# Optimization experiments

Measured on AMD Instinct MI355X. Metric: run time of the kernel, lower is better.

Reference implementation:

```python
import jax, jax.numpy as jnp
import numpy as np

B, S, D = 4, 2048, 1024
N_HEAD = 16
HEAD_DIM = D // N_HEAD


def setup_inputs() -> dict:
    key = jax.random.key(0)
    k1, k2, k3 = jax.random.split(key, 3)
    std = 0.02
    return {
        "x": jax.random.normal(k1, (B, S, D), dtype=jnp.float32),
        "c_attn_w": jax.random.normal(k2, (D, 3 * D), dtype=jnp.float32) * std,
        "c_attn_b": jnp.zeros((3 * D,), dtype=jnp.float32),
        "c_proj_w": jax.random.normal(k3, (D, D), dtype=jnp.float32) * std,
        "c_proj_b": jnp.zeros((D,), dtype=jnp.float32),
    }


def _split_heads(t):
    # [B, S, D] -> [B, H, S, hd]
    b, s, d = t.shape
    return t.reshape(b, s, N_HEAD, d // N_HEAD).transpose(0, 2, 1, 3)


def reference(x, c_attn_w, c_attn_b, c_proj_w, c_proj_b):
    # fused QKV projection (TFConv1D = x @ w + b)
    qkv = x @ c_attn_w + c_attn_b                      # [B, S, 3D]
    q, k, v = jnp.split(qkv, 3, axis=2)
    q, k, v = _split_heads(q), _split_heads(k), _split_heads(v)  # [B, H, S, hd]

    # scaled scores
    w = jnp.einsum('bhqd,bhkd->bhqk', q, k)
    w = w / jnp.sqrt(jnp.asarray(HEAD_DIM, w.dtype))

    # causal mask via multiplicative trick: i >= j - ns + nd (nd == ns == S)
    nd = ns = S
    i = jnp.arange(nd)[:, None]
    j = jnp.arange(ns)[None, :]
    b = (i >= j - ns + nd).astype(w.dtype)[None, None]  # [1,1,nd,ns]
    w = w * b - 10000.0 * (1.0 - b)

    w = jax.nn.softmax(w, axis=-1)
    a = jnp.einsum('bhqk,bhkd->bhqd', w, v)            # [B, H, S, hd]

    # merge heads: [B, H, S, hd] -> [B, S, D]
    a = a.transpose(0, 2, 1, 3).reshape(x.shape[0], x.shape[1], -1)
    a = a @ c_proj_w + c_proj_b
    return a
```

## Files before the change

### kernel.cpp

```cpp
#include <hip/hip_runtime.h>
#include <hip/hip_bf16.h>

typedef unsigned short ushort_t;
typedef __attribute__((ext_vector_type(8))) short short8;
typedef __attribute__((ext_vector_type(4))) float floatx4;

#define LOG2E 1.4426950408889634f

__device__ __forceinline__ unsigned short f2bf(float f) {
    unsigned u = __float_as_uint(f);
    u += 0x7FFF + ((u >> 16) & 1);
    return (unsigned short)(u >> 16);
}

__device__ __forceinline__ void async_ld16(const void* gptr, void* lptr) {
    typedef const __attribute__((address_space(1))) unsigned int TG;
    typedef __attribute__((address_space(3))) unsigned int TL;
    __builtin_amdgcn_global_load_lds((TG*)(unsigned long long)gptr,
                                     (TL*)(unsigned)(unsigned long long)lptr,
                                     16, 0, 0);
}

__global__ __launch_bounds__(256) void cvt_bf16_kernel(const float* __restrict__ in,
                                                       ushort_t* __restrict__ out, int n4) {
    int i = blockIdx.x * 256 + threadIdx.x;
    if (i >= n4) return;
    float4 v = ((const float4*)in)[i];
    unsigned long long r = (unsigned long long)f2bf(v.x)
                         | ((unsigned long long)f2bf(v.y) << 16)
                         | ((unsigned long long)f2bf(v.z) << 32)
                         | ((unsigned long long)f2bf(v.w) << 48);
    ((unsigned long long*)out)[i] = r;
}

__global__ __launch_bounds__(256) void transpose_cvt_kernel(const float* __restrict__ in,
                                                            ushort_t* __restrict__ out,
                                                            int R, int C) {
    __shared__ float t[32][33];
    int nbc = C >> 5;
    int bc = blockIdx.x % nbc, br = blockIdx.x / nbc;
    int tx = threadIdx.x & 31, ty = threadIdx.x >> 5;
    int r0 = br << 5, c0 = bc << 5;
#pragma unroll
    for (int j = 0; j < 4; ++j)
        t[ty + j * 8][tx] = in[(size_t)(r0 + ty + j * 8) * C + c0 + tx];
    __syncthreads();
#pragma unroll
    for (int j = 0; j < 4; ++j)
        out[(size_t)(c0 + ty + j * 8) * R + r0 + tx] = f2bf(t[tx][ty + j * 8]);
}

__global__ __launch_bounds__(256) void gemm_qkv_kernel(const ushort_t* __restrict__ A,
                                                       const ushort_t* __restrict__ Bt,
                                                       const float* __restrict__ bias,
                                                       ushort_t* __restrict__ qbuf,
                                                       ushort_t* __restrict__ kbuf,
                                                       ushort_t* __restrict__ vtbuf) {
    const int K = 1024, nbn = 24;
    __shared__ __align__(16) ushort_t As[128 * 32];
    __shared__ __align__(16) ushort_t Bs[128 * 32];
    int bm = blockIdx.x / nbn, bn = blockIdx.x % nbn;
    int m0 = bm << 7, n0 = bn << 7;
    int tid = threadIdx.x;
    int wave = tid >> 6, lane = tid & 63;
    int c = lane & 15, g = lane >> 4;
    int m_off = (wave & 1) << 6, n_off = (wave >> 1) << 6;
    int ldrow = lane >> 2;
    int ldk   = (lane & 3) << 3;

    floatx4 acc[4][4];
#pragma unroll
    for (int mi = 0; mi < 4; ++mi)
#pragma unroll
        for (int ni = 0; ni < 4; ++ni) {
            floatx4 z = {0.f, 0.f, 0.f, 0.f};
            acc[mi][ni] = z;
        }

    for (int kk = 0; kk < K; kk += 32) {
        __syncthreads();
#pragma unroll
        for (int j = 0; j < 2; ++j) {
            int chunk = wave * 2 + j;
            async_ld16(A  + (size_t)(m0 + chunk * 16 + ldrow) * K + kk + ldk, &As[chunk * 512]);
            async_ld16(Bt + (size_t)(n0 + chunk * 16 + ldrow) * K + kk + ldk, &Bs[chunk * 512]);
        }
        __syncthreads();
        short8 bf[4];
#pragma unroll
        for (int ni = 0; ni < 4; ++ni)
            bf[ni] = *(const short8*)&Bs[(n_off + ni * 16 + c) * 32 + g * 8];
#pragma unroll
        for (int mi = 0; mi < 4; ++mi) {
            short8 af = *(const short8*)&As[(m_off + mi * 16 + c) * 32 + g * 8];
#pragma unroll
            for (int ni = 0; ni < 4; ++ni)
                acc[mi][ni] = __builtin_amdgcn_mfma_f32_16x16x32_bf16(af, bf[ni], acc[mi][ni], 0, 0, 0);
        }
    }

    int sec = n0 >> 10;
    float scl = (sec == 0) ? (0.125f * LOG2E) : 1.0f;
    float bv[4]; int hh[4], dd[4];
#pragma unroll
    for (int ni = 0; ni < 4; ++ni) {
        int coln = n0 + n_off + ni * 16 + c;
        bv[ni] = bias[coln];
        int coll = coln & 1023;
        hh[ni] = coll >> 6; dd[ni] = coll & 63;
    }
#pragma unroll
    for (int mi = 0; mi < 4; ++mi) {
        int rowb = m0 + m_off + mi * 16 + g * 4;
        int bb = rowb >> 11, sbase = rowb & 2047;
#pragma unroll
        for (int ni = 0; ni < 4; ++ni) {
            size_t bhn = (size_t)(bb * 16 + hh[ni]);
            if (sec == 2) {
                unsigned long long pk = 0;
#pragma unroll
                for (int r = 0; r < 4; ++r)
                    pk |= (unsigned long long)f2bf(acc[mi][ni][r] + bv[ni]) << (16 * r);
                *(unsigned long long*)(vtbuf + bhn * 131072 + (size_t)dd[ni] * 2048 + sbase) = pk;
            } else {
                ushort_t* dst = (sec == 0 ? qbuf : kbuf) + (bhn * 2048 + sbase) * 64 + dd[ni];
#pragma unroll
                for (int r = 0; r < 4; ++r)
                    dst[r * 64] = f2bf((acc[mi][ni][r] + bv[ni]) * scl);
            }
        }
    }
}

__global__ __launch_bounds__(256) void attn_kernel(const ushort_t* __restrict__ qb_,
                                                   const ushort_t* __restrict__ kb_,
                                                   const ushort_t* __restrict__ vtb_,
                                                   ushort_t* __restrict__ aout) {
    __shared__ __align__(16) ushort_t Ks[128 * 72];
    __shared__ __align__(16) ushort_t Vs[64 * 136];
    __shared__ __align__(16) ushort_t Ps[4][16 * 136];
    int bx = blockIdx.x;
    int qb = 15 - (bx >> 6);
    int bhix = bx & 63;
    int b = bhix >> 4, h = bhix & 15;
    int q0 = qb << 7;
    int tid = threadIdx.x, wave = tid >> 6, lane = tid & 63;
    int c = lane & 15, g = lane >> 4;
    size_t bh = (size_t)(b * 16 + h);

    const ushort_t* Qp = qb_ + (bh * 2048 + q0) * 64;
    const ushort_t* Kp = kb_ + bh * 131072;
    const ushort_t* Vp = vtb_ + bh * 131072;

    short8 qf[2][2];
#pragma unroll
    for (int ss = 0; ss < 2; ++ss) {
        int qr = (wave * 2 + ss) * 16 + c;
        qf[ss][0] = *(const short8*)(Qp + qr * 64 + g * 8);
        qf[ss][1] = *(const short8*)(Qp + qr * 64 + 32 + g * 8);
    }

    float l_part[2] = {0.f, 0.f};
    floatx4 o_acc[2][4];
#pragma unroll
    for (int ss = 0; ss < 2; ++ss)
#pragma unroll
        for (int nt = 0; nt < 4; ++nt) { floatx4 z = {0.f,0.f,0.f,0.f}; o_acc[ss][nt] = z; }

    short8 kreg[4], vreg[4];
#pragma unroll
    for (int it = 0; it < 4; ++it) {
        int idx = it * 256 + tid;
        kreg[it] = *(const short8*)(Kp + idx * 8);
        vreg[it] = *(const short8*)(Vp + (idx >> 4) * 2048 + (idx & 15) * 8);
    }

    for (int kt = 0; kt <= qb; ++kt) {
        int kt0 = kt << 7;
        __syncthreads();
#pragma unroll
        for (int it = 0; it < 4; ++it) {
            int idx = it * 256 + tid;
            *(short8*)&Ks[(idx >> 3) * 72 + (idx & 7) * 8] = kreg[it];
            *(short8*)&Vs[(idx >> 4) * 136 + (idx & 15) * 8] = vreg[it];
        }
        __syncthreads();
        if (kt < qb) {
            int s0 = (kt + 1) << 7;
#pragma unroll
            for (int it = 0; it < 4; ++it) {
                int idx = it * 256 + tid;
                kreg[it] = *(const short8*)(Kp + s0 * 64 + idx * 8);
                vreg[it] = *(const short8*)(Vp + (idx >> 4) * 2048 + s0 + (idx & 15) * 8);
            }
        }
        bool diag = (kt == qb);

#pragma unroll
        for (int ss = 0; ss < 2; ++ss) {
            int rl0 = (wave * 2 + ss) * 16;
            floatx4 sacc[8];
#pragma unroll
            for (int nt = 0; nt < 8; ++nt) {
                floatx4 z = {0.f, 0.f, 0.f, 0.f};
                short8 kf0 = *(const short8*)&Ks[(nt * 16 + c) * 72 + g * 8];
                z = __builtin_amdgcn_mfma_f32_16x16x32_bf16(kf0, qf[ss][0], z, 0, 0, 0);
                short8 kf1 = *(const short8*)&Ks[(nt * 16 + c) * 72 + 32 + g * 8];
                sacc[nt] = __builtin_amdgcn_mfma_f32_16x16x32_bf16(kf1, qf[ss][1], z, 0, 0, 0);
            }

            int qg = q0 + rl0 + c;
            float lp = 0.f;
#pragma unroll
            for (int nt = 0; nt < 8; ++nt) {
                float p[4];
#pragma unroll
                for (int r = 0; r < 4; ++r) {
                    float s = sacc[nt][r];
                    if (diag) {
                        int kp = kt0 + nt * 16 + g * 4 + r;
                        s = (kp > qg) ? -1e30f : s;
                    }
                    p[r] = exp2f(s);
                    lp += p[r];
                }
                union { unsigned long long u; __hip_bfloat162 h[2]; } pk;
                pk.h[0] = __float22bfloat162_rn(make_float2(p[0], p[1]));
                pk.h[1] = __float22bfloat162_rn(make_float2(p[2], p[3]));
                *(unsigned long long*)&Ps[wave][c * 136 + nt * 16 + g * 4] = pk.u;
            }
            l_part[ss] += lp;

#pragma unroll
            for (int ks = 0; ks < 4; ++ks) {
                short8 pf = *(const short8*)&Ps[wave][c * 136 + ks * 32 + g * 8];
#pragma unroll
                for (int nt = 0; nt < 4; ++nt) {
                    short8 vf = *(const short8*)&Vs[(nt * 16 + c) * 136 + ks * 32 + g * 8];
                    o_acc[ss][nt] = __builtin_amdgcn_mfma_f32_16x16x32_bf16(pf, vf, o_acc[ss][nt], 0, 0, 0);
                }
            }
        }
    }

#pragma unroll
    for (int ss = 0; ss < 2; ++ss) {
        float l = l_part[ss];
        l += __shfl_xor(l, 16);
        l += __shfl_xor(l, 32);
        float linv = 1.0f / l;
        float inv[4];
#pragma unroll
        for (int r = 0; r < 4; ++r)
            inv[r] = __shfl(linv, g * 4 + r);
#pragma unroll
        for (int nt = 0; nt < 4; ++nt)
#pragma unroll
            for (int r = 0; r < 4; ++r) {
                int q = q0 + (wave * 2 + ss) * 16 + g * 4 + r;
                aout[(size_t)(b * 2048 + q) * 1024 + h * 64 + nt * 16 + c] =
                    f2bf(o_acc[ss][nt][r] * inv[r]);
            }
    }
}

__global__ __launch_bounds__(256) void gemm_proj_kernel(const ushort_t* __restrict__ A,
                                                        const ushort_t* __restrict__ Bt,
                                                        const float* __restrict__ bias,
                                                        float* __restrict__ Cout) {
    const int K = 1024, N = 1024, nbn = 8;
    __shared__ __align__(16) ushort_t As[128 * 32];
    __shared__ __align__(16) ushort_t Bs[128 * 32];
    int bm = blockIdx.x / nbn, bn = blockIdx.x % nbn;
    int m0 = bm << 7, n0 = bn << 7;
    int tid = threadIdx.x;
    int wave = tid >> 6, lane = tid & 63;
    int c = lane & 15, g = lane >> 4;
    int m_off = (wave & 1) << 6, n_off = (wave >> 1) << 6;
    int ldrow = lane >> 2;
    int ldk   = (lane & 3) << 3;

    floatx4 acc[4][4];
#pragma unroll
    for (int mi = 0; mi < 4; ++mi)
#pragma unroll
        for (int ni = 0; ni < 4; ++ni) {
            floatx4 z = {0.f, 0.f, 0.f, 0.f};
            acc[mi][ni] = z;
        }

    for (int kk = 0; kk < K; kk += 32) {
        __syncthreads();
#pragma unroll
        for (int j = 0; j < 2; ++j) {
            int chunk = wave * 2 + j;
            async_ld16(A  + (size_t)(m0 + chunk * 16 + ldrow) * K + kk + ldk, &As[chunk * 512]);
            async_ld16(Bt + (size_t)(n0 + chunk * 16 + ldrow) * K + kk + ldk, &Bs[chunk * 512]);
        }
        __syncthreads();
        short8 bf[4];
#pragma unroll
        for (int ni = 0; ni < 4; ++ni)
            bf[ni] = *(const short8*)&Bs[(n_off + ni * 16 + c) * 32 + g * 8];
#pragma unroll
        for (int mi = 0; mi < 4; ++mi) {
            short8 af = *(const short8*)&As[(m_off + mi * 16 + c) * 32 + g * 8];
#pragma unroll
            for (int ni = 0; ni < 4; ++ni)
                acc[mi][ni] = __builtin_amdgcn_mfma_f32_16x16x32_bf16(af, bf[ni], acc[mi][ni], 0, 0, 0);
        }
    }

    float bv[4];
#pragma unroll
    for (int ni = 0; ni < 4; ++ni) bv[ni] = bias[n0 + n_off + ni * 16 + c];
#pragma unroll
    for (int mi = 0; mi < 4; ++mi)
#pragma unroll
        for (int ni = 0; ni < 4; ++ni)
#pragma unroll
            for (int r = 0; r < 4; ++r) {
                int row = m0 + m_off + mi * 16 + g * 4 + r;
                int col = n0 + n_off + ni * 16 + c;
                Cout[(size_t)row * N + col] = acc[mi][ni][r] + bv[ni];
            }
}

extern "C" void kernel_launch(void* const* d_in, const int* in_sizes, int n_in,
                              void* d_out, int out_size, void* d_ws, size_t ws_size,
                              hipStream_t stream) {
    const float* x        = (const float*)d_in[0];
    const float* c_attn_w = (const float*)d_in[1];
    const float* c_attn_b = (const float*)d_in[2];
    const float* c_proj_w = (const float*)d_in[3];
    const float* c_proj_b = (const float*)d_in[4];
    float* out = (float*)d_out;

    char* ws = (char*)d_ws;
    ushort_t* xb     = (ushort_t*)(ws);
    ushort_t* wqkvT  = (ushort_t*)(ws + 16777216);
    ushort_t* wprojT = (ushort_t*)(ws + 23068672);
    ushort_t* qbuf   = (ushort_t*)(ws + 25165824);
    ushort_t* kbuf   = (ushort_t*)(ws + 41943040);
    ushort_t* vtbuf  = (ushort_t*)(ws + 58720256);

    cvt_bf16_kernel<<<8192, 256, 0, stream>>>(x, xb, 2097152);
    transpose_cvt_kernel<<<32 * 96, 256, 0, stream>>>(c_attn_w, wqkvT, 1024, 3072);
    transpose_cvt_kernel<<<32 * 32, 256, 0, stream>>>(c_proj_w, wprojT, 1024, 1024);
    gemm_qkv_kernel<<<64 * 24, 256, 0, stream>>>(xb, wqkvT, c_attn_b, qbuf, kbuf, vtbuf);
    attn_kernel<<<1024, 256, 0, stream>>>(qbuf, kbuf, vtbuf, xb);
    gemm_proj_kernel<<<64 * 8, 256, 0, stream>>>(xb, wprojT, c_proj_b, out);
}
```

Measured before the change: 296.8 us.

## Merge prep conversion kernels and interleave both query subtiles in attention QK loop

The three preprocessing launches (x to bf16, and the two weight transposes with conversion) are merged into one kernel that dispatches on block index, removing two launch gaps. In the attention kernel, the two 16-row query subtiles now share each K fragment load from LDS and their QK MFMAs are interleaved. The second subtile's packed probabilities are held in registers and written to the P buffer after the first subtile's PV pass. This halves K reads from shared memory and exposes more independent MFMAs, at the cost of extra registers that may lower occupancy.

```diff
diff --git a/kernel.cpp b/kernel.cpp
--- a/kernel.cpp
+++ b/kernel.cpp
@@ -21,24 +21,29 @@
                                      16, 0, 0);
 }
 
-__global__ __launch_bounds__(256) void cvt_bf16_kernel(const float* __restrict__ in,
-                                                       ushort_t* __restrict__ out, int n4) {
-    int i = blockIdx.x * 256 + threadIdx.x;
-    if (i >= n4) return;
-    float4 v = ((const float4*)in)[i];
-    unsigned long long r = (unsigned long long)f2bf(v.x)
-                         | ((unsigned long long)f2bf(v.y) << 16)
-                         | ((unsigned long long)f2bf(v.z) << 32)
-                         | ((unsigned long long)f2bf(v.w) << 48);
-    ((unsigned long long*)out)[i] = r;
-}
-
-__global__ __launch_bounds__(256) void transpose_cvt_kernel(const float* __restrict__ in,
-                                                            ushort_t* __restrict__ out,
-                                                            int R, int C) {
+__global__ __launch_bounds__(256) void prep_kernel(const float* __restrict__ x,
+                                                   const float* __restrict__ wqkv,
+                                                   const float* __restrict__ wproj,
+                                                   ushort_t* __restrict__ xb,
+                                                   ushort_t* __restrict__ wqkvT,
+                                                   ushort_t* __restrict__ wprojT) {
     __shared__ float t[32][33];
+    int bx = blockIdx.x;
+    if (bx < 8192) {
+        int i = bx * 256 + threadIdx.x;
+        float4 v = ((const float4*)x)[i];
+        unsigned long long r = (unsigned long long)f2bf(v.x)
+                             | ((unsigned long long)f2bf(v.y) << 16)
+                             | ((unsigned long long)f2bf(v.z) << 32)
+                             | ((unsigned long long)f2bf(v.w) << 48);
+        ((unsigned long long*)xb)[i] = r;
+        return;
+    }
+    const float* in; ushort_t* out; int R, C, bidx;
+    if (bx < 8192 + 3072) { in = wqkv; out = wqkvT; R = 1024; C = 3072; bidx = bx - 8192; }
+    else                  { in = wproj; out = wprojT; R = 1024; C = 1024; bidx = bx - 11264; }
     int nbc = C >> 5;
-    int bc = blockIdx.x % nbc, br = blockIdx.x / nbc;
+    int bc = bidx % nbc, br = bidx / nbc;
     int tx = threadIdx.x & 31, ty = threadIdx.x >> 5;
     int r0 = br << 5, c0 = bc << 5;
 #pragma unroll
@@ -175,6 +180,7 @@
         vreg[it] = *(const short8*)(Vp + (idx >> 4) * 2048 + (idx & 15) * 8);
     }
 
+    int qg0 = q0 + wave * 32 + c;
     for (int kt = 0; kt <= qb; ++kt) {
         int kt0 = kt << 7;
         __syncthreads();
@@ -196,49 +202,65 @@
         }
         bool diag = (kt == qb);
 
-#pragma unroll
-        for (int ss = 0; ss < 2; ++ss) {
-            int rl0 = (wave * 2 + ss) * 16;
-            floatx4 sacc[8];
-#pragma unroll
-            for (int nt = 0; nt < 8; ++nt) {
-                floatx4 z = {0.f, 0.f, 0.f, 0.f};
-                short8 kf0 = *(const short8*)&Ks[(nt * 16 + c) * 72 + g * 8];
-                z = __builtin_amdgcn_mfma_f32_16x16x32_bf16(kf0, qf[ss][0], z, 0, 0, 0);
-                short8 kf1 = *(const short8*)&Ks[(nt * 16 + c) * 72 + 32 + g * 8];
-                sacc[nt] = __builtin_amdgcn_mfma_f32_16x16x32_bf16(kf1, qf[ss][1], z, 0, 0, 0);
-            }
-
-            int qg = q0 + rl0 + c;
-            float lp = 0.f;
-#pragma unroll
-            for (int nt = 0; nt < 8; ++nt) {
-                float p[4];
-#pragma unroll
-                for (int r = 0; r < 4; ++r) {
-                    float s = sacc[nt][r];
-                    if (diag) {
-                        int kp = kt0 + nt * 16 + g * 4 + r;
-                        s = (kp > qg) ? -1e30f : s;
-                    }
-                    p[r] = exp2f(s);
-                    lp += p[r];
+        unsigned pd[8][2];
+        float lp0 = 0.f, lp1 = 0.f;
+#pragma unroll
+        for (int nt = 0; nt < 8; ++nt) {
+            short8 kf0 = *(const short8*)&Ks[(nt * 16 + c) * 72 + g * 8];
+            short8 kf1 = *(const short8*)&Ks[(nt * 16 + c) * 72 + 32 + g * 8];
+            floatx4 z0 = {0.f, 0.f, 0.f, 0.f};
+            z0 = __builtin_amdgcn_mfma_f32_16x16x32_bf16(kf0, qf[0][0], z0, 0, 0, 0);
+            z0 = __builtin_amdgcn_mfma_f32_16x16x32_bf16(kf1, qf[0][1], z0, 0, 0, 0);
+            floatx4 z1 = {0.f, 0.f, 0.f, 0.f};
+            z1 = __builtin_amdgcn_mfma_f32_16x16x32_bf16(kf0, qf[1][0], z1, 0, 0, 0);
+            z1 = __builtin_amdgcn_mfma_f32_16x16x32_bf16(kf1, qf[1][1], z1, 0, 0, 0);
+
+            int kpb = kt0 + nt * 16 + g * 4;
+            float p0[4], p1[4];
+#pragma unroll
+            for (int r = 0; r < 4; ++r) {
+                float s0v = z0[r], s1v = z1[r];
+                if (diag) {
+                    int kp = kpb + r;
+                    s0v = (kp > qg0)      ? -1e30f : s0v;
+                    s1v = (kp > qg0 + 16) ? -1e30f : s1v;
                 }
-                union { unsigned long long u; __hip_bfloat162 h[2]; } pk;
-                pk.h[0] = __float22bfloat162_rn(make_float2(p[0], p[1]));
-                pk.h[1] = __float22bfloat162_rn(make_float2(p[2], p[3]));
-                *(unsigned long long*)&Ps[wave][c * 136 + nt * 16 + g * 4] = pk.u;
-            }
-            l_part[ss] += lp;
-
-#pragma unroll
-            for (int ks = 0; ks < 4; ++ks) {
-                short8 pf = *(const short8*)&Ps[wave][c * 136 + ks * 32 + g * 8];
-#pragma unroll
-                for (int nt = 0; nt < 4; ++nt) {
-                    short8 vf = *(const short8*)&Vs[(nt * 16 + c) * 136 + ks * 32 + g * 8];
-                    o_acc[ss][nt] = __builtin_amdgcn_mfma_f32_16x16x32_bf16(pf, vf, o_acc[ss][nt], 0, 0, 0);
-                }
+                p0[r] = exp2f(s0v); lp0 += p0[r];
+                p1[r] = exp2f(s1v); lp1 += p1[r];
+            }
+            union { unsigned long long u; __hip_bfloat162 h[2]; unsigned w[2]; } pk;
+            pk.h[0] = __float22bfloat162_rn(make_float2(p0[0], p0[1]));
+            pk.h[1] = __float22bfloat162_rn(make_float2(p0[2], p0[3]));
+            *(unsigned long long*)&Ps[wave][c * 136 + nt * 16 + g * 4] = pk.u;
+            pk.h[0] = __float22bfloat162_rn(make_float2(p1[0], p1[1]));
+            pk.h[1] = __float22bfloat162_rn(make_float2(p1[2], p1[3]));
+            pd[nt][0] = pk.w[0]; pd[nt][1] = pk.w[1];
+        }
+        l_part[0] += lp0;
+        l_part[1] += lp1;
+
+#pragma unroll
+        for (int ks = 0; ks < 4; ++ks) {
+            short8 pf = *(const short8*)&Ps[wave][c * 136 + ks * 32 + g * 8];
+#pragma unroll
+            for (int nt = 0; nt < 4; ++nt) {
+                short8 vf = *(const short8*)&Vs[(nt * 16 + c) * 136 + ks * 32 + g * 8];
+                o_acc[0][nt] = __builtin_amdgcn_mfma_f32_16x16x32_bf16(pf, vf, o_acc[0][nt], 0, 0, 0);
+            }
+        }
+#pragma unroll
+        for (int nt = 0; nt < 8; ++nt) {
+            union { unsigned long long u; unsigned w[2]; } pk;
+            pk.w[0] = pd[nt][0]; pk.w[1] = pd[nt][1];
+            *(unsigned long long*)&Ps[wave][c * 136 + nt * 16 + g * 4] = pk.u;
+        }
+#pragma unroll
+        for (int ks = 0; ks < 4; ++ks) {
+            short8 pf = *(const short8*)&Ps[wave][c * 136 + ks * 32 + g * 8];
+#pragma unroll
+            for (int nt = 0; nt < 4; ++nt) {
+                short8 vf = *(const short8*)&Vs[(nt * 16 + c) * 136 + ks * 32 + g * 8];
+                o_acc[1][nt] = __builtin_amdgcn_mfma_f32_16x16x32_bf16(pf, vf, o_acc[1][nt], 0, 0, 0);
             }
         }
     }
@@ -344,9 +366,7 @@
     ushort_t* kbuf   = (ushort_t*)(ws + 41943040);
     ushort_t* vtbuf  = (ushort_t*)(ws + 58720256);
 
-    cvt_bf16_kernel<<<8192, 256, 0, stream>>>(x, xb, 2097152);
-    transpose_cvt_kernel<<<32 * 96, 256, 0, stream>>>(c_attn_w, wqkvT, 1024, 3072);
-    transpose_cvt_kernel<<<32 * 32, 256, 0, stream>>>(c_proj_w, wprojT, 1024, 1024);
+    prep_kernel<<<12288, 256, 0, stream>>>(x, c_attn_w, c_proj_w, xb, wqkvT, wprojT);
     gemm_qkv_kernel<<<64 * 24, 256, 0, stream>>>(xb, wqkvT, c_attn_b, qbuf, kbuf, vtbuf);
     attn_kernel<<<1024, 256, 0, stream>>>(qbuf, kbuf, vtbuf, xb);
     gemm_proj_kernel<<<64 * 8, 256, 0, stream>>>(xb, wprojT, c_proj_b, out);
```

Measured after the change: 292.3 us. No clear change (-1.5%).
